# Kernel tuning notes

Measured on AMD Instinct MI355X. Metric: run time of the kernel, lower is better.

## Reference

```python
import jax, jax.numpy as jnp
from jax import lax
import numpy as np

B, T, D, H, O = 128, 256, 512, 1024, 1024


def setup_inputs() -> dict:
    key = jax.random.key(0)
    ks = jax.random.split(key, 6)
    s = 0.02
    x = jax.random.normal(ks[0], (B, T, D), dtype=jnp.float32)
    # Gates stacked in order (i, f, g, o). Each gate in the original has three
    # biases (W_x*.bias + W_h*.bias + b_*); their sum is equivalent to the
    # single per-gate bias b below (same function space).
    Wx = jax.random.normal(ks[1], (4, H, D), dtype=jnp.float32) * s
    Wh = jax.random.normal(ks[2], (4, H, H), dtype=jnp.float32) * s
    b = jax.random.normal(ks[3], (4, H), dtype=jnp.float32) * s
    Whp = jax.random.normal(ks[4], (O, H), dtype=jnp.float32) * s
    bhp = jax.random.normal(ks[5], (O,), dtype=jnp.float32) * s
    return {"x": x, "Wx": Wx, "Wh": Wh, "b": b, "Whp": Whp, "bhp": bhp}


def reference(x, Wx, Wh, b, Whp, bhp):
    batch = x.shape[0]
    hid = Wh.shape[-1]
    # Precompute all input projections in one big GEMM: [B,T,4,H]
    xproj = jnp.einsum('btd,ghd->btgh', x, Wx) + b

    def step(carry, xp_t):
        h, c = carry
        # xp_t: [B,4,H]; recurrent projection for all 4 gates in one GEMM
        gates = xp_t + jnp.einsum('bk,gok->bgo', h, Wh)
        i_t = jax.nn.sigmoid(gates[:, 0])
        f_t = jax.nn.sigmoid(gates[:, 1])
        g_t = jnp.tanh(gates[:, 2])
        o_t = jax.nn.sigmoid(gates[:, 3])
        c = f_t * c + i_t * g_t
        h = o_t * jnp.tanh(c)
        return (h, c), None

    h0 = jnp.zeros((batch, hid), dtype=x.dtype)
    c0 = jnp.zeros((batch, hid), dtype=x.dtype)
    (h_T, _), _ = lax.scan(step, (h0, c0), jnp.swapaxes(xproj, 0, 1))
    logits = h_T @ Whp.T + bhp
    return jax.nn.softmax(logits, axis=1)
```

## Files before the change

### kernel.cpp

```cpp
#include <hip/hip_runtime.h>

#define B_ 128
#define T_ 256
#define D_ 512
#define H_ 1024
#define O_ 1024
#define NWG 256
#define NCOL 32

typedef _Float16 f16;
typedef _Float16 f16x8 __attribute__((ext_vector_type(8)));
typedef float f32x4 __attribute__((ext_vector_type(4)));

#define HSTEP 131072ull

#define OFF_XH   0ull
#define SZ_XH    33554432ull
#define OFF_WHPK (OFF_XH + SZ_XH)
#define SZ_WHPK  8388608ull
#define OFF_WXPK (OFF_WHPK + SZ_WHPK)
#define SZ_WXPK  4194304ull
#define OFF_BIAS (OFF_WXPK + SZ_WXPK)
#define SZ_BIAS  16384ull
#define OFF_H    (OFF_BIAS + SZ_BIAS)
#define SZ_H     (2ull * HSTEP * (T_ + 1))
#define OFF_WHPT (OFF_H + SZ_H)
#define SZ_WHPT  4194304ull
#define OFF_BAR  (OFF_WHPT + SZ_WHPT)

__device__ __forceinline__ void st_h16(f16* p, f16x8 v)
{
    asm volatile("global_store_dwordx4 %0, %1, off sc0 sc1"
                 :: "v"(p), "v"(v) : "memory");
}

__device__ __forceinline__ int ld_flag(const int* p)
{
    int r;
    asm volatile("global_load_dword %0, %1, off sc0 sc1\n\t"
                 "s_waitcnt vmcnt(0)"
                 : "=v"(r) : "v"(p) : "memory");
    return r;
}


__global__ __launch_bounds__(256, 1)
void pack_x(const float* __restrict__ x, f16* __restrict__ xh)
{
    const int id = blockIdx.x * 256 + threadIdx.x;
    const int doct = id & 63;
    const int t = (id >> 6) & 255;
    const int b = id >> 14;
    const float* src = x + ((size_t)b * T_ + t) * D_ + (doct << 3);
    const float4 v0 = *(const float4*)src;
    const float4 v1 = *(const float4*)(src + 4);
    f16x8 o;
    o[0] = (f16)v0.x; o[1] = (f16)v0.y; o[2] = (f16)v0.z; o[3] = (f16)v0.w;
    o[4] = (f16)v1.x; o[5] = (f16)v1.y; o[6] = (f16)v1.z; o[7] = (f16)v1.w;
    *(f16x8*)(xh + ((((size_t)t << 6) + doct) * B_ + b) * 8) = o;
}

__global__ __launch_bounds__(256, 1)
void pack_wh(const float* __restrict__ Wh, f16* __restrict__ whpk)
{
    const int id = blockIdx.x * 256 + threadIdx.x;
    const int n = id & 31;
    const int koct = (id >> 5) & 127;
    const int w = id >> 12;
    const int g = n >> 3;
    const int o = (w << 3) + (n & 7);
    const float* src = Wh + ((size_t)g * H_ + o) * H_ + (koct << 3);
    const float4 v0 = *(const float4*)src;
    const float4 v1 = *(const float4*)(src + 4);
    f16x8 ov;
    ov[0] = (f16)v0.x; ov[1] = (f16)v0.y; ov[2] = (f16)v0.z; ov[3] = (f16)v0.w;
    ov[4] = (f16)v1.x; ov[5] = (f16)v1.y; ov[6] = (f16)v1.z; ov[7] = (f16)v1.w;
    *(f16x8*)(whpk + (size_t)id * 8) = ov;
}

__global__ __launch_bounds__(256, 1)
void pack_wx(const float* __restrict__ Wx, f16* __restrict__ wxpk)
{
    const int id = blockIdx.x * 256 + threadIdx.x;
    const int n = id & 31;
    const int doct = (id >> 5) & 63;
    const int w = id >> 11;
    const int g = n >> 3;
    const int o = (w << 3) + (n & 7);
    const float* src = Wx + ((size_t)g * H_ + o) * D_ + (doct << 3);
    const float4 v0 = *(const float4*)src;
    const float4 v1 = *(const float4*)(src + 4);
    f16x8 ov;
    ov[0] = (f16)v0.x; ov[1] = (f16)v0.y; ov[2] = (f16)v0.z; ov[3] = (f16)v0.w;
    ov[4] = (f16)v1.x; ov[5] = (f16)v1.y; ov[6] = (f16)v1.z; ov[7] = (f16)v1.w;
    *(f16x8*)(wxpk + (size_t)id * 8) = ov;
}

__global__ __launch_bounds__(256, 1)
void pack_bias(const float* __restrict__ bsrc, float* __restrict__ biasp)
{
    const int id = blockIdx.x * 256 + threadIdx.x;
    const int n = id & 31;
    const int w = id >> 5;
    biasp[id] = bsrc[((size_t)(n >> 3) << 10) + (w << 3) + (n & 7)];
}

__global__ __launch_bounds__(256, 1)
void whp_t(const float* __restrict__ Whp, float* __restrict__ wT)
{
    __shared__ float tile[64][65];
    const int bx = blockIdx.x & 15;
    const int by = blockIdx.x >> 4;
    for (int i = threadIdx.x; i < 4096; i += 256) {
        const int r = i >> 6, c = i & 63;
        tile[r][c] = Whp[((size_t)(by * 64 + r) << 10) + bx * 64 + c];
    }
    __syncthreads();
    for (int i = threadIdx.x; i < 4096; i += 256) {
        const int r = i >> 6, c = i & 63;
        wT[((size_t)(bx * 64 + r) << 10) + by * 64 + c] = tile[c][r];
    }
}

__global__ __launch_bounds__(1024, 1)
void lstm_loop(const f16* __restrict__ xh,
               const f16* __restrict__ whpk,
               const f16* __restrict__ wxpk,
               const float* __restrict__ biasp,
               f16* __restrict__ hbuf,
               int* __restrict__ bar)
{
    __shared__ f16   lds_wh[(H_/8) * NCOL * 8];
    __shared__ f16   lds_wx[(D_/8) * NCOL * 8];
    __shared__ float lds_red[3][4][8][64];
    __shared__ f16   lds_hst[64 * 8];

    const int tid = threadIdx.x;
    const int w = blockIdx.x;
    const int dom = w >> 7;
    const int wc = w & 127;

    {
        const f16x8* s1 = (const f16x8*)(whpk + (size_t)wc * (H_/8) * NCOL * 8);
        f16x8* d1 = (f16x8*)lds_wh;
        for (int i = tid; i < (H_/8) * NCOL; i += 1024) d1[i] = s1[i];
        const f16x8* s2 = (const f16x8*)(wxpk + (size_t)wc * (D_/8) * NCOL * 8);
        f16x8* d2 = (f16x8*)lds_wx;
        for (int i = tid; i < (D_/8) * NCOL; i += 1024) d2[i] = s2[i];
    }
    __syncthreads();

    const int lane = tid & 63;
    const int wv = tid >> 6;
    const int kq = wv >> 2;
    const int rg = wv & 3;
    const int quad = lane >> 4;
    const int l16 = lane & 15;
    const int mrow = (dom << 6) + (rg << 4) + l16;
    const int last = (kq == 3);

    const float b0r = biasp[wc * NCOL + l16];
    const float b1r = biasp[wc * NCOL + 16 + l16];
    const float i0 = last ? b0r : 0.f;
    const float i1 = last ? b1r : 0.f;

    float cs0 = 0.f, cs1 = 0.f;
    const int hi = (l16 >> 3) & 1;
    const int r0 = hi << 1;
    const int oc = l16 & 7;
    const int rowbase = (rg << 4) + (quad << 2) + r0;

    const int* __restrict__ fq = bar + (dom << 7) + (kq << 5) + (lane & 31);

    for (int t = 0; t < T_; ++t) {
        const f16* __restrict__ hr = hbuf + (size_t)t * HSTEP;
        f16* hw = hbuf + (size_t)(t + 1) * HSTEP;

        f32x4 acc0 = {i0, i0, i0, i0};
        f32x4 acc1 = {i1, i1, i1, i1};

        const f16* __restrict__ xt = xh + (size_t)t * (D_/8) * B_ * 8;
        {
            f16x8 XA[4];
            #pragma unroll
            for (int kc = 0; kc < 4; ++kc) {
                const int doct = (kq << 4) + (kc << 2) + quad;
                XA[kc] = *(const f16x8*)(xt + (((size_t)doct << 7) + mrow) * 8);
            }
            #pragma unroll
            for (int kc = 0; kc < 4; ++kc) {
                const int doct = (kq << 4) + (kc << 2) + quad;
                f16x8 b0 = *(const f16x8*)(lds_wx + ((doct << 5) + l16) * 8);
                f16x8 b1 = *(const f16x8*)(lds_wx + ((doct << 5) + 16 + l16) * 8);
                acc0 = __builtin_amdgcn_mfma_f32_16x16x32_f16(XA[kc], b0, acc0, 0, 0, 0);
                acc1 = __builtin_amdgcn_mfma_f32_16x16x32_f16(XA[kc], b1, acc1, 0, 0, 0);
            }
        }

        if (t) {
            while (!__all(ld_flag(fq) >= t))
                __builtin_amdgcn_s_sleep(1);
        }

        {
            f16x8 A[8];
            #pragma unroll
            for (int kc = 0; kc < 8; ++kc) {
                const int koct = (kq << 5) + (kc << 2) + quad;
                A[kc] = *(const f16x8*)(hr + (((size_t)koct << 7) + mrow) * 8);
            }
            #pragma unroll
            for (int kc = 0; kc < 8; ++kc) {
                const int koct = (kq << 5) + (kc << 2) + quad;
                f16x8 b0 = *(const f16x8*)(lds_wh + ((koct << 5) + l16) * 8);
                f16x8 b1 = *(const f16x8*)(lds_wh + ((koct << 5) + 16 + l16) * 8);
                acc0 = __builtin_amdgcn_mfma_f32_16x16x32_f16(A[kc], b0, acc0, 0, 0, 0);
                acc1 = __builtin_amdgcn_mfma_f32_16x16x32_f16(A[kc], b1, acc1, 0, 0, 0);
            }
        }

        if (!last) {
            #pragma unroll
            for (int r = 0; r < 4; ++r) {
                lds_red[kq][rg][r][lane]     = acc0[r];
                lds_red[kq][rg][4 + r][lane] = acc1[r];
            }
        }
        __syncthreads();

        if (last) {
            #pragma unroll
            for (int q = 0; q < 3; ++q) {
                #pragma unroll
                for (int r = 0; r < 4; ++r) {
                    acc0[r] += lds_red[q][rg][r][lane];
                    acc1[r] += lds_red[q][rg][4 + r][lane];
                }
            }
            f32x4 p0, p1;
            #pragma unroll
            for (int r = 0; r < 4; ++r) {
                p0[r] = __shfl_xor(acc0[r], 8, 64);
                p1[r] = __shfl_xor(acc1[r], 8, 64);
            }
            #pragma unroll
            for (int i = 0; i < 2; ++i) {
                const int r = r0 + i;
                const float gi = hi ? p0[r]   : acc0[r];
                const float gf = hi ? acc0[r] : p0[r];
                const float gg = hi ? p1[r]   : acc1[r];
                const float go = hi ? acc1[r] : p1[r];
                const float it = 1.0f / (1.0f + __expf(-gi));
                const float ft = 1.0f / (1.0f + __expf(-gf));
                const float eg = __expf(2.0f * gg);
                const float gt = 1.0f - 2.0f / (eg + 1.0f);
                const float ot = 1.0f / (1.0f + __expf(-go));
                float c = (i == 0) ? cs0 : cs1;
                c = ft * c + it * gt;
                if (i == 0) cs0 = c; else cs1 = c;
                const float ec = __expf(2.0f * c);
                const float tc = 1.0f - 2.0f / (ec + 1.0f);
                lds_hst[((rowbase + i) << 3) + oc] = (f16)(ot * tc);
            }
        }
        __syncthreads();

        if (tid < 64) {
            f16x8 v = *(const f16x8*)(lds_hst + (tid << 3));
            st_h16(hw + ((size_t)(wc << 7) + (dom << 6) + tid) * 8, v);
            asm volatile("s_waitcnt vmcnt(0)" ::: "memory");
            if (tid == 0)
                __hip_atomic_store(bar + w, t + 1, __ATOMIC_RELAXED, __HIP_MEMORY_SCOPE_AGENT);
        }
    }
}

__global__ __launch_bounds__(256, 1)
void finale(const f16* __restrict__ hT,
            const float* __restrict__ whpT,
            const float* __restrict__ bhp,
            float* __restrict__ outp)
{
    __shared__ float hrow[H_];
    __shared__ float red[16];
    const int tid = threadIdx.x;
    const int b = blockIdx.x;

    if (tid < H_/8) {
        f16x8 v = *(const f16x8*)(hT + (((size_t)tid << 7) + b) * 8);
        #pragma unroll
        for (int j = 0; j < 8; ++j) hrow[(tid << 3) + j] = (float)v[j];
    }
    __syncthreads();

    float lg0 = bhp[tid], lg1 = bhp[tid + 256], lg2 = bhp[tid + 512], lg3 = bhp[tid + 768];
    for (int k = 0; k < H_; ++k) {
        const float hv = hrow[k];
        const float* wr = whpT + ((size_t)k << 10);
        lg0 = fmaf(hv, wr[tid],       lg0);
        lg1 = fmaf(hv, wr[tid + 256], lg1);
        lg2 = fmaf(hv, wr[tid + 512], lg2);
        lg3 = fmaf(hv, wr[tid + 768], lg3);
    }

    const int lane = tid & 63, wv = tid >> 6;
    float mx = fmaxf(fmaxf(lg0, lg1), fmaxf(lg2, lg3));
    for (int off = 32; off > 0; off >>= 1) mx = fmaxf(mx, __shfl_down(mx, off, 64));
    if (lane == 0) red[wv] = mx;
    __syncthreads();
    mx = fmaxf(fmaxf(red[0], red[1]), fmaxf(red[2], red[3]));

    const float e0 = __expf(lg0 - mx), e1 = __expf(lg1 - mx);
    const float e2 = __expf(lg2 - mx), e3 = __expf(lg3 - mx);
    float s = e0 + e1 + e2 + e3;
    for (int off = 32; off > 0; off >>= 1) s += __shfl_down(s, off, 64);
    if (lane == 0) red[8 + wv] = s;
    __syncthreads();
    s = red[8] + red[9] + red[10] + red[11];
    const float inv = 1.0f / s;

    float* op = outp + ((size_t)b << 10);
    op[tid]       = e0 * inv;
    op[tid + 256] = e1 * inv;
    op[tid + 512] = e2 * inv;
    op[tid + 768] = e3 * inv;
}

extern "C" void kernel_launch(void* const* d_in, const int* in_sizes, int n_in,
                              void* d_out, int out_size, void* d_ws, size_t ws_size,
                              hipStream_t stream)
{
    const float* x    = (const float*)d_in[0];
    const float* Wx   = (const float*)d_in[1];
    const float* Wh   = (const float*)d_in[2];
    const float* bias = (const float*)d_in[3];
    const float* Whp  = (const float*)d_in[4];
    const float* bhp  = (const float*)d_in[5];

    char* ws = (char*)d_ws;
    f16*   xh    = (f16*)(ws + OFF_XH);
    f16*   whpk  = (f16*)(ws + OFF_WHPK);
    f16*   wxpk  = (f16*)(ws + OFF_WXPK);
    float* biasp = (float*)(ws + OFF_BIAS);
    f16*   hbuf  = (f16*)(ws + OFF_H);
    float* whpT  = (float*)(ws + OFF_WHPT);
    int*   bar   = (int*)(ws + OFF_BAR);

    hipMemsetAsync(ws + OFF_H, 0, 2ull * HSTEP, stream);
    hipMemsetAsync(ws + OFF_BAR, 0, 1024, stream);

    pack_x   <<<8192, 256, 0, stream>>>(x, xh);
    pack_wh  <<<2048, 256, 0, stream>>>(Wh, whpk);
    pack_wx  <<<1024, 256, 0, stream>>>(Wx, wxpk);
    pack_bias<<<16,   256, 0, stream>>>(bias, biasp);
    whp_t    <<<256,  256, 0, stream>>>(Whp, whpT);

    lstm_loop<<<NWG, 1024, 0, stream>>>(xh, whpk, wxpk, biasp, hbuf, bar);
    finale   <<<B_,  256, 0, stream>>>(hbuf + (size_t)T_ * HSTEP, whpT, bhp, (float*)d_out);
}
```

Baseline: 1.204 ms.

## Publish h directly per wave with per-row-group flags and prefetch next x

Removes the LDS staging of h and the extra block barrier before the store. Each final-stage wave now writes its h values straight to global memory with 2-byte stores and publishes its own per-row-group progress flag, so consumers wait only on the row group they need. The input slice for the next timestep is also prefetched into registers during the current step. The trade-off is many narrow scattered stores instead of one wide store per lane, 4x more flags to poll, and an added barrier after the reduction.

```diff
diff --git a/kernel.cpp b/kernel.cpp
--- a/kernel.cpp
+++ b/kernel.cpp
@@ -28,9 +28,9 @@
 #define SZ_WHPT  4194304ull
 #define OFF_BAR  (OFF_WHPT + SZ_WHPT)
 
-__device__ __forceinline__ void st_h16(f16* p, f16x8 v)
-{
-    asm volatile("global_store_dwordx4 %0, %1, off sc0 sc1"
+__device__ __forceinline__ void st_h2(f16* p, unsigned int v)
+{
+    asm volatile("global_store_short %0, %1, off sc0 sc1"
                  :: "v"(p), "v"(v) : "memory");
 }
 
@@ -133,7 +133,6 @@
     __shared__ f16   lds_wh[(H_/8) * NCOL * 8];
     __shared__ f16   lds_wx[(D_/8) * NCOL * 8];
     __shared__ float lds_red[3][4][8][64];
-    __shared__ f16   lds_hst[64 * 8];
 
     const int tid = threadIdx.x;
     const int w = blockIdx.x;
@@ -170,7 +169,16 @@
     const int oc = l16 & 7;
     const int rowbase = (rg << 4) + (quad << 2) + r0;
 
-    const int* __restrict__ fq = bar + (dom << 7) + (kq << 5) + (lane & 31);
+    const int* __restrict__ fq =
+        bar + (dom << 9) + (((kq << 5) + (lane & 31)) << 2) + rg;
+    int* __restrict__ fpub = bar + (dom << 9) + (wc << 2) + rg;
+
+    f16x8 XA[4];
+    #pragma unroll
+    for (int kc = 0; kc < 4; ++kc) {
+        const int doct = (kq << 4) + (kc << 2) + quad;
+        XA[kc] = *(const f16x8*)(xh + (((size_t)doct << 7) + mrow) * 8);
+    }
 
     for (int t = 0; t < T_; ++t) {
         const f16* __restrict__ hr = hbuf + (size_t)t * HSTEP;
@@ -179,21 +187,21 @@
         f32x4 acc0 = {i0, i0, i0, i0};
         f32x4 acc1 = {i1, i1, i1, i1};
 
-        const f16* __restrict__ xt = xh + (size_t)t * (D_/8) * B_ * 8;
-        {
-            f16x8 XA[4];
+        #pragma unroll
+        for (int kc = 0; kc < 4; ++kc) {
+            const int doct = (kq << 4) + (kc << 2) + quad;
+            f16x8 b0 = *(const f16x8*)(lds_wx + ((doct << 5) + l16) * 8);
+            f16x8 b1 = *(const f16x8*)(lds_wx + ((doct << 5) + 16 + l16) * 8);
+            acc0 = __builtin_amdgcn_mfma_f32_16x16x32_f16(XA[kc], b0, acc0, 0, 0, 0);
+            acc1 = __builtin_amdgcn_mfma_f32_16x16x32_f16(XA[kc], b1, acc1, 0, 0, 0);
+        }
+
+        if (t + 1 < T_) {
+            const f16* __restrict__ xtn = xh + (size_t)(t + 1) * (D_/8) * B_ * 8;
             #pragma unroll
             for (int kc = 0; kc < 4; ++kc) {
                 const int doct = (kq << 4) + (kc << 2) + quad;
-                XA[kc] = *(const f16x8*)(xt + (((size_t)doct << 7) + mrow) * 8);
-            }
-            #pragma unroll
-            for (int kc = 0; kc < 4; ++kc) {
-                const int doct = (kq << 4) + (kc << 2) + quad;
-                f16x8 b0 = *(const f16x8*)(lds_wx + ((doct << 5) + l16) * 8);
-                f16x8 b1 = *(const f16x8*)(lds_wx + ((doct << 5) + 16 + l16) * 8);
-                acc0 = __builtin_amdgcn_mfma_f32_16x16x32_f16(XA[kc], b0, acc0, 0, 0, 0);
-                acc1 = __builtin_amdgcn_mfma_f32_16x16x32_f16(XA[kc], b1, acc1, 0, 0, 0);
+                XA[kc] = *(const f16x8*)(xtn + (((size_t)doct << 7) + mrow) * 8);
             }
         }
 
@@ -237,6 +245,10 @@
                     acc1[r] += lds_red[q][rg][4 + r][lane];
                 }
             }
+        }
+        __syncthreads();
+
+        if (last) {
             f32x4 p0, p1;
             #pragma unroll
             for (int r = 0; r < 4; ++r) {
@@ -260,17 +272,14 @@
                 if (i == 0) cs0 = c; else cs1 = c;
                 const float ec = __expf(2.0f * c);
                 const float tc = 1.0f - 2.0f / (ec + 1.0f);
-                lds_hst[((rowbase + i) << 3) + oc] = (f16)(ot * tc);
-            }
-        }
-        __syncthreads();
-
-        if (tid < 64) {
-            f16x8 v = *(const f16x8*)(lds_hst + (tid << 3));
-            st_h16(hw + ((size_t)(wc << 7) + (dom << 6) + tid) * 8, v);
+                union { f16 h; unsigned short u; } cv;
+                cv.h = (f16)(ot * tc);
+                st_h2(hw + ((size_t)(wc << 7) + (dom << 6) + rowbase + i) * 8 + oc,
+                      (unsigned int)cv.u);
+            }
             asm volatile("s_waitcnt vmcnt(0)" ::: "memory");
-            if (tid == 0)
-                __hip_atomic_store(bar + w, t + 1, __ATOMIC_RELAXED, __HIP_MEMORY_SCOPE_AGENT);
+            if (lane == 0)
+                __hip_atomic_store(fpub, t + 1, __ATOMIC_RELAXED, __HIP_MEMORY_SCOPE_AGENT);
         }
     }
 }
@@ -347,7 +356,7 @@
     int*   bar   = (int*)(ws + OFF_BAR);
 
     hipMemsetAsync(ws + OFF_H, 0, 2ull * HSTEP, stream);
-    hipMemsetAsync(ws + OFF_BAR, 0, 1024, stream);
+    hipMemsetAsync(ws + OFF_BAR, 0, 4096, stream);
 
     pack_x   <<<8192, 256, 0, stream>>>(x, xh);
     pack_wh  <<<2048, 256, 0, stream>>>(Wh, whpk);
```

Measured after the change: 2.674 ms. +122.1%, slower.
